# Performance work log

Measured on AMD Instinct MI355X. Metric: run time of the kernel, lower is better.

## Reference

```python
import jax, jax.numpy as jnp
import numpy as np

BETA = 0.5
IGNORE_INDEX = -100
TEMPERATURE = 1.0

N, H, V = 2048, 4096, 32000


def setup_inputs() -> dict:
    key = jax.random.key(0)
    k1, k2, k3, k4, k5 = jax.random.split(key, 5)
    scale_s = 1.0 / np.sqrt(H // 2)
    scale_t = 1.0 / np.sqrt(H)
    return {
        "student": jax.random.normal(k1, (N, H // 2), dtype=jnp.float32),
        "W_s": jax.random.normal(k2, (V, H // 2), dtype=jnp.float32) * scale_s,
        "teacher": jax.random.normal(k3, (N, H), dtype=jnp.float32),
        "W_t": jax.random.normal(k4, (V, H), dtype=jnp.float32) * scale_t,
        "target": jax.random.randint(k5, (N,), 0, V, dtype=jnp.int64),
    }


def reference(student, W_s, teacher, W_t, target):
    # Fused linear + JSD: logits are [N, V] (the huge intermediates Liger avoids
    # materializing by chunking over N).
    s_logits = (student @ W_s.T) / TEMPERATURE          # [N, V]  student -> Q
    t_logits = (teacher @ W_t.T) / TEMPERATURE          # [N, V]  teacher -> P
    log_q = jax.nn.log_softmax(s_logits, axis=-1)
    log_p = jax.nn.log_softmax(t_logits, axis=-1)
    p = jnp.exp(log_p)
    q = jnp.exp(log_q)
    # Generalized JSD(beta): beta*KL(P||M) + (1-beta)*KL(Q||M), M = beta*P + (1-beta)*Q
    m = BETA * p + (1.0 - BETA) * q
    log_m = jnp.log(m)
    per_tok = (BETA * jnp.sum(p * (log_p - log_m), axis=-1)
               + (1.0 - BETA) * jnp.sum(q * (log_q - log_m), axis=-1))  # [N]
    mask = target != IGNORE_INDEX
    n_non_ignore = jnp.maximum(jnp.sum(mask), 1)
    loss = jnp.sum(jnp.where(mask, per_tok, 0.0)) / n_non_ignore.astype(per_tok.dtype)
    return loss
```

## Files before the change

kernel.cpp:

```cpp
#include <hip/hip_runtime.h>
#include <hip/hip_bf16.h>
#include <hip/hip_fp8.h>
#include <stdint.h>

#define BETA 0.5f
#define IGNORE_INDEX (-100)
#define WSCALE 64.0f
#define INV_WSCALE 0.015625f

typedef float f32x4 __attribute__((ext_vector_type(4)));
typedef long longx2 __attribute__((ext_vector_type(2)));

__global__ __launch_bounds__(256) void f32_to_fp8_kernel(
    const float* __restrict__ in, uint8_t* __restrict__ out, int n, float scale) {
  int i = (blockIdx.x * blockDim.x + threadIdx.x) * 8;
  const int stride = gridDim.x * blockDim.x * 8;
  for (; i < n; i += stride) {
    float4 v0 = *reinterpret_cast<const float4*>(in + i);
    float4 v1 = *reinterpret_cast<const float4*>(in + i + 4);
    const float f[8] = {v0.x, v0.y, v0.z, v0.w, v1.x, v1.y, v1.z, v1.w};
    union { uint8_t b[8]; uint2 u; } o;
#pragma unroll
    for (int j = 0; j < 8; ++j) {
      __hip_fp8_e4m3 h(f[j] * scale);
      o.b[j] = h.__x;
    }
    *reinterpret_cast<uint2*>(out + i) = o.u;
  }
}


__global__ __launch_bounds__(512, 2) void gemm_f8q_kernel(
    const uint8_t* __restrict__ At, const uint8_t* __restrict__ Bt,
    uint16_t* __restrict__ Ct, int Kt,
    const uint8_t* __restrict__ As_, const uint8_t* __restrict__ Bs_,
    uint16_t* __restrict__ Cs, int Ks,
    int V, int RT, int CT) {
  __shared__ __align__(16) uint8_t lds[65536];

  const int half = RT * CT;
  const uint8_t *A, *B;
  uint16_t* C;
  int K, bidx = blockIdx.x;
  if (bidx < half) { A = At; B = Bt; C = Ct; K = Kt; }
  else             { A = As_; B = Bs_; C = Cs; K = Ks; bidx -= half; }

  int L = ((half & 7) == 0) ? ((bidx & 7) * (half >> 3) + (bidx >> 3)) : bidx;
  const int rt = L % RT;
  const int ct = L / RT;
  const int row0 = rt * 256;
  const int col0 = ct * 256;

  const int i  = threadIdx.x;
  const int w  = i >> 6;
  const int l  = i & 63;
  const int wl = l & 15;
  const int kg = l >> 4;
  const int wr = w >> 2;
  const int wc = w & 3;

  const int nT = K >> 6;

  const int rg = i >> 2;
  const int pq = i & 3;
  const int qlog = pq ^ ((rg >> 1) & 3);
  const uint8_t* aSrc = A + (size_t)(row0 + rg) * K + qlog * 16;
  const uint8_t* bSrc = B + (size_t)(col0 + rg) * K + qlog * 16;
  uint8_t* ldsu = lds;

#define GL(srcp, dstp)                                                     \
  __builtin_amdgcn_global_load_lds(                                        \
      (const __attribute__((address_space(1))) void*)(srcp),               \
      (__attribute__((address_space(3))) void*)(dstp), 16, 0, 0)

#define STAGE_A(TT)                                                        \
  do {                                                                     \
    const uint8_t* _s = aSrc + (size_t)(TT) * 64;                          \
    uint8_t* _d = ldsu + (((TT) & 1) * 32768) + i * 16;                    \
    GL(_s, _d); GL(_s + (size_t)128 * K, _d + 8192);                       \
  } while (0)

#define STAGE_B(TT)                                                        \
  do {                                                                     \
    const uint8_t* _s = bSrc + (size_t)(TT) * 64;                          \
    uint8_t* _d = ldsu + (((TT) & 1) * 32768) + 16384 + i * 16;            \
    GL(_s, _d); GL(_s + (size_t)128 * K, _d + 8192);                       \
  } while (0)

  int offA[8], offB[4];
  const int qsw = (kg ^ ((wl >> 1) & 3)) * 16;
#pragma unroll
  for (int m = 0; m < 8; ++m) {
    const int r = wr * 128 + m * 16 + wl;
    offA[m] = r * 64 + qsw;
  }
#pragma unroll
  for (int n = 0; n < 4; ++n) {
    const int r = wc * 64 + n * 16 + wl;
    offB[n] = 16384 + r * 64 + qsw;
  }

  f32x4 acc[8][4] = {};
  longx2 af[4], ag[4], bf[4];

  STAGE_A(0); STAGE_B(0);
  if (nT > 1) {
    STAGE_B(1);
    asm volatile("s_waitcnt vmcnt(2)" ::: "memory");
  } else {
    asm volatile("s_waitcnt vmcnt(0)" ::: "memory");
  }
  __builtin_amdgcn_s_barrier();
  __builtin_amdgcn_sched_barrier(0);

  for (int T = 0; T < nT; ++T) {
    const uint8_t* bb = lds + (T & 1) * 32768;
    const bool stg1 = (T + 1) < nT;
    const bool stg2 = (T + 2) < nT;

#pragma unroll
    for (int m = 0; m < 4; ++m)
      af[m] = *reinterpret_cast<const longx2*>(bb + offA[m]);
#pragma unroll
    for (int n = 0; n < 4; ++n)
      bf[n] = *reinterpret_cast<const longx2*>(bb + offB[n]);
    if (stg1) STAGE_A(T + 1);
    __builtin_amdgcn_s_setprio(1);
#pragma unroll
    for (int m = 0; m < 4; ++m)
#pragma unroll
      for (int n = 0; n < 4; ++n)
        acc[m][n] = __builtin_amdgcn_mfma_f32_16x16x32_fp8_fp8(
            af[m][0], bf[n][0], acc[m][n], 0, 0, 0);
    __builtin_amdgcn_s_setprio(0);

#pragma unroll
    for (int m = 0; m < 4; ++m)
      ag[m] = *reinterpret_cast<const longx2*>(bb + offA[4 + m]);
    __builtin_amdgcn_s_setprio(1);
#pragma unroll
    for (int m = 0; m < 4; ++m)
#pragma unroll
      for (int n = 0; n < 4; ++n)
        acc[4 + m][n] = __builtin_amdgcn_mfma_f32_16x16x32_fp8_fp8(
            ag[m][0], bf[n][0], acc[4 + m][n], 0, 0, 0);
    __builtin_amdgcn_s_setprio(0);

    if (stg2) STAGE_B(T + 2);
    __builtin_amdgcn_s_setprio(1);
#pragma unroll
    for (int m = 0; m < 4; ++m)
#pragma unroll
      for (int n = 0; n < 4; ++n)
        acc[m][n] = __builtin_amdgcn_mfma_f32_16x16x32_fp8_fp8(
            af[m][1], bf[n][1], acc[m][n], 0, 0, 0);
    __builtin_amdgcn_s_setprio(0);

    __builtin_amdgcn_s_setprio(1);
#pragma unroll
    for (int m = 0; m < 4; ++m)
#pragma unroll
      for (int n = 0; n < 4; ++n)
        acc[4 + m][n] = __builtin_amdgcn_mfma_f32_16x16x32_fp8_fp8(
            ag[m][1], bf[n][1], acc[4 + m][n], 0, 0, 0);
    __builtin_amdgcn_s_setprio(0);

    if (stg2) {
      asm volatile("s_waitcnt vmcnt(2)" ::: "memory");
    } else {
      asm volatile("s_waitcnt vmcnt(0)" ::: "memory");
    }
    __builtin_amdgcn_s_barrier();
    __builtin_amdgcn_sched_barrier(0);
  }

#pragma unroll
  for (int mg = 0; mg < 8; ++mg)
#pragma unroll
    for (int ng = 0; ng < 4; ++ng)
#pragma unroll
      for (int r = 0; r < 4; ++r) {
        const int row = row0 + wr * 128 + mg * 16 + kg * 4 + r;
        const int col = col0 + wc * 64 + ng * 16 + wl;
        __hip_bfloat16 bv = __float2bfloat16(acc[mg][ng][r] * INV_WSCALE);
        C[(size_t)row * V + col] = *reinterpret_cast<const uint16_t*>(&bv);
      }
#undef STAGE_A
#undef STAGE_B
#undef GL
}

__device__ __forceinline__ void unpack8(uint4 v, float* f) {
  uint32_t w[4] = {v.x, v.y, v.z, v.w};
#pragma unroll
  for (int j = 0; j < 4; ++j) {
    union { uint32_t u; float x; } lo, hi;
    lo.u = (w[j] & 0xffffu) << 16;
    hi.u = w[j] & 0xffff0000u;
    f[2 * j] = lo.x;
    f[2 * j + 1] = hi.x;
  }
}

__device__ __forceinline__ float blockReduce(float v, float* sh) {
#pragma unroll
  for (int o = 32; o >= 1; o >>= 1) v += __shfl_xor(v, o, 64);
  const int w = threadIdx.x >> 6;
  __syncthreads();
  if ((threadIdx.x & 63) == 0) sh[w] = v;
  __syncthreads();
  float r = sh[0];
#pragma unroll
  for (int i = 1; i < 4; ++i) r += sh[i];
  return r;
}

__global__ __launch_bounds__(256) void jsd_rows_kernel(
    const uint16_t* __restrict__ SL, const uint16_t* __restrict__ TL,
    float* __restrict__ per_tok, int V) {
  __shared__ __align__(16) uint16_t rowS[32000];
  __shared__ __align__(16) uint16_t rowT[32000];
  __shared__ float redM[2][4], redS[2][4], red[4];

  const int t = threadIdx.x;
  const int row = blockIdx.x;
  const uint4* gS = reinterpret_cast<const uint4*>(SL + (size_t)row * V);
  const uint4* gT = reinterpret_cast<const uint4*>(TL + (size_t)row * V);
  uint4* lS = reinterpret_cast<uint4*>(rowS);
  uint4* lT = reinterpret_cast<uint4*>(rowT);
  const int nvec = V >> 3;

  float mS = -3.0e38f, sS = 0.f, mT = -3.0e38f, sT = 0.f;
  for (int i = t; i < nvec; i += 256) {
    uint4 vs = gS[i], vt = gT[i];
    lS[i] = vs; lT[i] = vt;
    float fs[8], ft[8];
    unpack8(vs, fs);
    unpack8(vt, ft);
    float vmS = fs[0], vmT = ft[0];
#pragma unroll
    for (int j = 1; j < 8; ++j) { vmS = fmaxf(vmS, fs[j]); vmT = fmaxf(vmT, ft[j]); }
    if (vmS > mS) { sS *= __expf(mS - vmS); mS = vmS; }
    if (vmT > mT) { sT *= __expf(mT - vmT); mT = vmT; }
#pragma unroll
    for (int j = 0; j < 8; ++j) { sS += __expf(fs[j] - mS); sT += __expf(ft[j] - mT); }
  }

#pragma unroll
  for (int o = 32; o >= 1; o >>= 1) {
    float mo = __shfl_xor(mS, o, 64), so = __shfl_xor(sS, o, 64);
    float mn = fmaxf(mS, mo);
    sS = sS * __expf(mS - mn) + so * __expf(mo - mn); mS = mn;
    mo = __shfl_xor(mT, o, 64); so = __shfl_xor(sT, o, 64);
    mn = fmaxf(mT, mo);
    sT = sT * __expf(mT - mn) + so * __expf(mo - mn); mT = mn;
  }
  const int wv = t >> 6;
  if ((t & 63) == 0) {
    redM[0][wv] = mS; redS[0][wv] = sS;
    redM[1][wv] = mT; redS[1][wv] = sT;
  }
  __syncthreads();
  float M0 = redM[0][0], S0 = redS[0][0];
  float M1 = redM[1][0], S1 = redS[1][0];
#pragma unroll
  for (int k = 1; k < 4; ++k) {
    float m2 = redM[0][k], s2 = redS[0][k];
    float mn = fmaxf(M0, m2);
    S0 = S0 * __expf(M0 - mn) + s2 * __expf(m2 - mn); M0 = mn;
    m2 = redM[1][k]; s2 = redS[1][k];
    mn = fmaxf(M1, m2);
    S1 = S1 * __expf(M1 - mn) + s2 * __expf(m2 - mn); M1 = mn;
  }
  const float lseS = M0 + __logf(S0);
  const float lseT = M1 + __logf(S1);

  float acc = 0.f;
  for (int i = t; i < nvec; i += 256) {
    float fs[8], ft[8];
    unpack8(lS[i], fs);
    unpack8(lT[i], ft);
#pragma unroll
    for (int j = 0; j < 8; ++j) {
      const float lq = fs[j] - lseS;
      const float lp = ft[j] - lseT;
      const float q = __expf(lq);
      const float p = __expf(lp);
      const float m = BETA * p + (1.f - BETA) * q;
      const float lm = __logf(m);
      acc += BETA * p * (lp - lm) + (1.f - BETA) * q * (lq - lm);
    }
  }
  acc = blockReduce(acc, red);
  if (t == 0) per_tok[row] = acc;
}

__global__ __launch_bounds__(256) void finalize_kernel(
    const float* __restrict__ per_tok, const int* __restrict__ tgt,
    float* __restrict__ out, int N) {
  __shared__ float redf[4];
  __shared__ int redi[4];
  float s = 0.f;
  int c = 0;
  for (int i = threadIdx.x; i < N; i += 256) {
    if (tgt[i] != IGNORE_INDEX) { s += per_tok[i]; c += 1; }
  }
#pragma unroll
  for (int o = 32; o >= 1; o >>= 1) {
    s += __shfl_xor(s, o, 64);
    c += __shfl_xor(c, o, 64);
  }
  const int w = threadIdx.x >> 6;
  if ((threadIdx.x & 63) == 0) { redf[w] = s; redi[w] = c; }
  __syncthreads();
  if (threadIdx.x == 0) {
    float st = 0.f;
    int ct = 0;
#pragma unroll
    for (int i = 0; i < 4; ++i) { st += redf[i]; ct += redi[i]; }
    out[0] = st / (float)(ct > 0 ? ct : 1);
  }
}

extern "C" void kernel_launch(void* const* d_in, const int* in_sizes, int n_in,
                              void* d_out, int out_size, void* d_ws, size_t ws_size,
                              hipStream_t stream) {
  const float* student = (const float*)d_in[0];
  const float* W_s     = (const float*)d_in[1];
  const float* teacher = (const float*)d_in[2];
  const float* W_t     = (const float*)d_in[3];
  const int*   target  = (const int*)d_in[4];

  const int N  = in_sizes[4];
  const int Hs = in_sizes[0] / N;
  const int Ht = in_sizes[2] / N;
  const int V  = in_sizes[1] / Hs;

  char* ws = (char*)d_ws;
  size_t off = 0;
  auto alloc = [&](size_t bytes) -> void* {
    void* p = ws + off;
    off += (bytes + 255) & ~(size_t)255;
    return p;
  };
  uint8_t* Sf8  = (uint8_t*)alloc((size_t)N * Hs);
  uint8_t* Wsf8 = (uint8_t*)alloc((size_t)V * Hs);
  uint8_t* Tf8  = (uint8_t*)alloc((size_t)N * Ht);
  uint8_t* Wtf8 = (uint8_t*)alloc((size_t)V * Ht);
  uint16_t* slog = (uint16_t*)alloc((size_t)N * V * 2);
  uint16_t* tlog = (uint16_t*)alloc((size_t)N * V * 2);
  float* per_tok = (float*)alloc((size_t)N * sizeof(float));
  (void)ws_size;

  f32_to_fp8_kernel<<<512, 256, 0, stream>>>(student, Sf8, N * Hs, 1.0f);
  f32_to_fp8_kernel<<<2048, 256, 0, stream>>>(W_s, Wsf8, V * Hs, WSCALE);
  f32_to_fp8_kernel<<<512, 256, 0, stream>>>(teacher, Tf8, N * Ht, 1.0f);
  f32_to_fp8_kernel<<<2048, 256, 0, stream>>>(W_t, Wtf8, V * Ht, WSCALE);

  const int RT = N / 256;
  const int CT = V / 256;
  gemm_f8q_kernel<<<2 * RT * CT, 512, 0, stream>>>(
      Tf8, Wtf8, tlog, Ht, Sf8, Wsf8, slog, Hs, V, RT, CT);

  jsd_rows_kernel<<<N, 256, 0, stream>>>(slog, tlog, per_tok, V);
  finalize_kernel<<<1, 256, 0, stream>>>(per_tok, target, (float*)d_out, N);
}
```

Before: 874.1 us.

## Switch FP8 GEMM to scaled MFMA 16x16x128 with K=128 tiles

Replaces the 16x16x32 fp8 MFMA with the MI355 scaled MFMA (16x16x128 f8f6f4), doubling the K tile to 128 and LDS to 128KB double-buffered. The B-operand block scale is folded into the instruction (exponent 2^-6) so the epilogue no longer multiplies by 1/64. This cuts the MFMA instruction count and loop iterations, but the 128KB LDS limits occupancy to one block per CU despite launch_bounds(512,2).

```diff
diff --git a/kernel.cpp b/kernel.cpp
--- a/kernel.cpp
+++ b/kernel.cpp
@@ -6,10 +6,12 @@
 #define BETA 0.5f
 #define IGNORE_INDEX (-100)
 #define WSCALE 64.0f
-#define INV_WSCALE 0.015625f
+#define SCALE_ONE  0x7F7F7F7Fu
+#define SCALE_D64  0x79797979u
 
 typedef float f32x4 __attribute__((ext_vector_type(4)));
-typedef long longx2 __attribute__((ext_vector_type(2)));
+typedef int   i32x4 __attribute__((ext_vector_type(4)));
+typedef int   i32x8 __attribute__((ext_vector_type(8)));
 
 __global__ __launch_bounds__(256) void f32_to_fp8_kernel(
     const float* __restrict__ in, uint8_t* __restrict__ out, int n, float scale) {
@@ -30,13 +32,13 @@
 }
 
 
-__global__ __launch_bounds__(512, 2) void gemm_f8q_kernel(
+__global__ __launch_bounds__(512, 2) void gemm_mx_kernel(
     const uint8_t* __restrict__ At, const uint8_t* __restrict__ Bt,
     uint16_t* __restrict__ Ct, int Kt,
     const uint8_t* __restrict__ As_, const uint8_t* __restrict__ Bs_,
     uint16_t* __restrict__ Cs, int Ks,
     int V, int RT, int CT) {
-  __shared__ __align__(16) uint8_t lds[65536];
+  __shared__ __align__(16) uint8_t lds[131072];
 
   const int half = RT * CT;
   const uint8_t *A, *B;
@@ -59,13 +61,13 @@
   const int wr = w >> 2;
   const int wc = w & 3;
 
-  const int nT = K >> 6;
-
-  const int rg = i >> 2;
-  const int pq = i & 3;
-  const int qlog = pq ^ ((rg >> 1) & 3);
-  const uint8_t* aSrc = A + (size_t)(row0 + rg) * K + qlog * 16;
-  const uint8_t* bSrc = B + (size_t)(col0 + rg) * K + qlog * 16;
+  const int nT = K >> 7;
+
+  const int rg = i >> 3;
+  const int p8 = i & 7;
+  const int qsrc = p8 ^ (rg & 7);
+  const uint8_t* aSrc = A + (size_t)(row0 + rg) * K + qsrc * 16;
+  const uint8_t* bSrc = B + (size_t)(col0 + rg) * K + qsrc * 16;
   uint8_t* ldsu = lds;
 
 #define GL(srcp, dstp)                                                     \
@@ -75,38 +77,55 @@
 
 #define STAGE_A(TT)                                                        \
   do {                                                                     \
-    const uint8_t* _s = aSrc + (size_t)(TT) * 64;                          \
-    uint8_t* _d = ldsu + (((TT) & 1) * 32768) + i * 16;                    \
-    GL(_s, _d); GL(_s + (size_t)128 * K, _d + 8192);                       \
+    const uint8_t* _s = aSrc + (size_t)(TT) * 128;                         \
+    uint8_t* _d = ldsu + (((TT) & 1) * 65536) + i * 16;                    \
+    GL(_s, _d);                                                            \
+    GL(_s + (size_t)64 * K,  _d + 8192);                                   \
+    GL(_s + (size_t)128 * K, _d + 16384);                                  \
+    GL(_s + (size_t)192 * K, _d + 24576);                                  \
   } while (0)
 
 #define STAGE_B(TT)                                                        \
   do {                                                                     \
-    const uint8_t* _s = bSrc + (size_t)(TT) * 64;                          \
-    uint8_t* _d = ldsu + (((TT) & 1) * 32768) + 16384 + i * 16;            \
-    GL(_s, _d); GL(_s + (size_t)128 * K, _d + 8192);                       \
+    const uint8_t* _s = bSrc + (size_t)(TT) * 128;                         \
+    uint8_t* _d = ldsu + (((TT) & 1) * 65536) + 32768 + i * 16;            \
+    GL(_s, _d);                                                            \
+    GL(_s + (size_t)64 * K,  _d + 8192);                                   \
+    GL(_s + (size_t)128 * K, _d + 16384);                                  \
+    GL(_s + (size_t)192 * K, _d + 24576);                                  \
   } while (0)
 
-  int offA[8], offB[4];
-  const int qsw = (kg ^ ((wl >> 1) & 3)) * 16;
+  int offA[8][2], offB[4][2];
 #pragma unroll
   for (int m = 0; m < 8; ++m) {
     const int r = wr * 128 + m * 16 + wl;
-    offA[m] = r * 64 + qsw;
+#pragma unroll
+    for (int s = 0; s < 2; ++s)
+      offA[m][s] = r * 128 + (((2 * kg + s) ^ (wl & 7)) * 16);
   }
 #pragma unroll
   for (int n = 0; n < 4; ++n) {
     const int r = wc * 64 + n * 16 + wl;
-    offB[n] = 16384 + r * 64 + qsw;
+#pragma unroll
+    for (int s = 0; s < 2; ++s)
+      offB[n][s] = 32768 + r * 128 + (((2 * kg + s) ^ (wl & 7)) * 16);
   }
 
   f32x4 acc[8][4] = {};
-  longx2 af[4], ag[4], bf[4];
+  i32x8 aF[4], bF[4];
+
+#define LOADFRAG(dst, base, o0, o1)                                        \
+  do {                                                                     \
+    i32x4 _lo = *reinterpret_cast<const i32x4*>((base) + (o0));            \
+    i32x4 _hi = *reinterpret_cast<const i32x4*>((base) + (o1));            \
+    dst[0] = _lo[0]; dst[1] = _lo[1]; dst[2] = _lo[2]; dst[3] = _lo[3];    \
+    dst[4] = _hi[0]; dst[5] = _hi[1]; dst[6] = _hi[2]; dst[7] = _hi[3];    \
+  } while (0)
 
   STAGE_A(0); STAGE_B(0);
   if (nT > 1) {
     STAGE_B(1);
-    asm volatile("s_waitcnt vmcnt(2)" ::: "memory");
+    asm volatile("s_waitcnt vmcnt(4)" ::: "memory");
   } else {
     asm volatile("s_waitcnt vmcnt(0)" ::: "memory");
   }
@@ -114,59 +133,41 @@
   __builtin_amdgcn_sched_barrier(0);
 
   for (int T = 0; T < nT; ++T) {
-    const uint8_t* bb = lds + (T & 1) * 32768;
+    const uint8_t* bb = lds + (T & 1) * 65536;
     const bool stg1 = (T + 1) < nT;
     const bool stg2 = (T + 2) < nT;
 
 #pragma unroll
     for (int m = 0; m < 4; ++m)
-      af[m] = *reinterpret_cast<const longx2*>(bb + offA[m]);
+      LOADFRAG(aF[m], bb, offA[m][0], offA[m][1]);
 #pragma unroll
     for (int n = 0; n < 4; ++n)
-      bf[n] = *reinterpret_cast<const longx2*>(bb + offB[n]);
+      LOADFRAG(bF[n], bb, offB[n][0], offB[n][1]);
     if (stg1) STAGE_A(T + 1);
     __builtin_amdgcn_s_setprio(1);
 #pragma unroll
     for (int m = 0; m < 4; ++m)
 #pragma unroll
       for (int n = 0; n < 4; ++n)
-        acc[m][n] = __builtin_amdgcn_mfma_f32_16x16x32_fp8_fp8(
-            af[m][0], bf[n][0], acc[m][n], 0, 0, 0);
+        acc[m][n] = __builtin_amdgcn_mfma_scale_f32_16x16x128_f8f6f4(
+            aF[m], bF[n], acc[m][n], 0, 0, 0, SCALE_ONE, 0, SCALE_D64);
     __builtin_amdgcn_s_setprio(0);
 
 #pragma unroll
     for (int m = 0; m < 4; ++m)
-      ag[m] = *reinterpret_cast<const longx2*>(bb + offA[4 + m]);
-    __builtin_amdgcn_s_setprio(1);
-#pragma unroll
-    for (int m = 0; m < 4; ++m)
-#pragma unroll
-      for (int n = 0; n < 4; ++n)
-        acc[4 + m][n] = __builtin_amdgcn_mfma_f32_16x16x32_fp8_fp8(
-            ag[m][0], bf[n][0], acc[4 + m][n], 0, 0, 0);
-    __builtin_amdgcn_s_setprio(0);
-
+      LOADFRAG(aF[m], bb, offA[4 + m][0], offA[4 + m][1]);
     if (stg2) STAGE_B(T + 2);
     __builtin_amdgcn_s_setprio(1);
 #pragma unroll
     for (int m = 0; m < 4; ++m)
 #pragma unroll
       for (int n = 0; n < 4; ++n)
-        acc[m][n] = __builtin_amdgcn_mfma_f32_16x16x32_fp8_fp8(
-            af[m][1], bf[n][1], acc[m][n], 0, 0, 0);
+        acc[4 + m][n] = __builtin_amdgcn_mfma_scale_f32_16x16x128_f8f6f4(
+            aF[m], bF[n], acc[4 + m][n], 0, 0, 0, SCALE_ONE, 0, SCALE_D64);
     __builtin_amdgcn_s_setprio(0);
 
-    __builtin_amdgcn_s_setprio(1);
-#pragma unroll
-    for (int m = 0; m < 4; ++m)
-#pragma unroll
-      for (int n = 0; n < 4; ++n)
-        acc[4 + m][n] = __builtin_amdgcn_mfma_f32_16x16x32_fp8_fp8(
-            ag[m][1], bf[n][1], acc[4 + m][n], 0, 0, 0);
-    __builtin_amdgcn_s_setprio(0);
-
     if (stg2) {
-      asm volatile("s_waitcnt vmcnt(2)" ::: "memory");
+      asm volatile("s_waitcnt vmcnt(4)" ::: "memory");
     } else {
       asm volatile("s_waitcnt vmcnt(0)" ::: "memory");
     }
@@ -182,9 +183,10 @@
       for (int r = 0; r < 4; ++r) {
         const int row = row0 + wr * 128 + mg * 16 + kg * 4 + r;
         const int col = col0 + wc * 64 + ng * 16 + wl;
-        __hip_bfloat16 bv = __float2bfloat16(acc[mg][ng][r] * INV_WSCALE);
+        __hip_bfloat16 bv = __float2bfloat16(acc[mg][ng][r]);
         C[(size_t)row * V + col] = *reinterpret_cast<const uint16_t*>(&bv);
       }
+#undef LOADFRAG
 #undef STAGE_A
 #undef STAGE_B
 #undef GL
@@ -359,7 +361,7 @@
 
   const int RT = N / 256;
   const int CT = V / 256;
-  gemm_f8q_kernel<<<2 * RT * CT, 512, 0, stream>>>(
+  gemm_mx_kernel<<<2 * RT * CT, 512, 0, stream>>>(
       Tf8, Wtf8, tlog, Ht, Sf8, Wsf8, slog, Hs, V, RT, CT);
 
   jsd_rows_kernel<<<N, 256, 0, stream>>>(slog, tlog, per_tok, V);
```

Result: slower. 978.5 us (+11.9%).

## Switch FP8 GEMM to scaled 16x16x128 MFMA with four-stage LDS ring

Applied to the files above, without the earlier changes.

Replaces the 16x16x32 FP8 MFMA inner loop with the MI355X scaled MFMA (16x16x128 f8f6f4). Each instruction covers two 64-wide K tiles, and the weight scale of 1/64 is folded into the hardware scale operand instead of a multiply in the epilogue. LDS grows to 128KB to hold a four-buffer ring, and two tiles are prefetched per iteration. The aim is fewer MFMA issues at higher per-instruction throughput. In exchange, the larger LDS footprint likely limits occupancy to one block per CU despite launch bounds of 2, and the K-fragment packing across buffers has to match the new instruction's operand layout.

```diff
diff --git a/kernel.cpp b/kernel.cpp
--- a/kernel.cpp
+++ b/kernel.cpp
@@ -6,10 +6,12 @@
 #define BETA 0.5f
 #define IGNORE_INDEX (-100)
 #define WSCALE 64.0f
-#define INV_WSCALE 0.015625f
+#define SCALE_ONE  0x7F7F7F7Fu
+#define SCALE_D64  0x79797979u
 
 typedef float f32x4 __attribute__((ext_vector_type(4)));
-typedef long longx2 __attribute__((ext_vector_type(2)));
+typedef int   i32x4 __attribute__((ext_vector_type(4)));
+typedef int   i32x8 __attribute__((ext_vector_type(8)));
 
 __global__ __launch_bounds__(256) void f32_to_fp8_kernel(
     const float* __restrict__ in, uint8_t* __restrict__ out, int n, float scale) {
@@ -30,13 +32,13 @@
 }
 
 
-__global__ __launch_bounds__(512, 2) void gemm_f8q_kernel(
+__global__ __launch_bounds__(512, 2) void gemm_mx2_kernel(
     const uint8_t* __restrict__ At, const uint8_t* __restrict__ Bt,
     uint16_t* __restrict__ Ct, int Kt,
     const uint8_t* __restrict__ As_, const uint8_t* __restrict__ Bs_,
     uint16_t* __restrict__ Cs, int Ks,
     int V, int RT, int CT) {
-  __shared__ __align__(16) uint8_t lds[65536];
+  __shared__ __align__(16) uint8_t lds[131072];
 
   const int half = RT * CT;
   const uint8_t *A, *B;
@@ -59,7 +61,7 @@
   const int wr = w >> 2;
   const int wc = w & 3;
 
-  const int nT = K >> 6;
+  const int nJ = K >> 7;
 
   const int rg = i >> 2;
   const int pq = i & 3;
@@ -76,14 +78,14 @@
 #define STAGE_A(TT)                                                        \
   do {                                                                     \
     const uint8_t* _s = aSrc + (size_t)(TT) * 64;                          \
-    uint8_t* _d = ldsu + (((TT) & 1) * 32768) + i * 16;                    \
+    uint8_t* _d = ldsu + (((TT) & 3) * 32768) + i * 16;                    \
     GL(_s, _d); GL(_s + (size_t)128 * K, _d + 8192);                       \
   } while (0)
 
 #define STAGE_B(TT)                                                        \
   do {                                                                     \
     const uint8_t* _s = bSrc + (size_t)(TT) * 64;                          \
-    uint8_t* _d = ldsu + (((TT) & 1) * 32768) + 16384 + i * 16;            \
+    uint8_t* _d = ldsu + (((TT) & 3) * 32768) + 16384 + i * 16;            \
     GL(_s, _d); GL(_s + (size_t)128 * K, _d + 8192);                       \
   } while (0)
 
@@ -101,72 +103,53 @@
   }
 
   f32x4 acc[8][4] = {};
-  longx2 af[4], ag[4], bf[4];
-
-  STAGE_A(0); STAGE_B(0);
-  if (nT > 1) {
-    STAGE_B(1);
-    asm volatile("s_waitcnt vmcnt(2)" ::: "memory");
+  i32x8 bF[4];
+
+  STAGE_A(0); STAGE_B(0); STAGE_A(1); STAGE_B(1);
+  if (nJ > 1) {
+    STAGE_A(2); STAGE_B(2); STAGE_A(3); STAGE_B(3);
+    asm volatile("s_waitcnt vmcnt(8)" ::: "memory");
   } else {
     asm volatile("s_waitcnt vmcnt(0)" ::: "memory");
   }
   __builtin_amdgcn_s_barrier();
   __builtin_amdgcn_sched_barrier(0);
 
-  for (int T = 0; T < nT; ++T) {
-    const uint8_t* bb = lds + (T & 1) * 32768;
-    const bool stg1 = (T + 1) < nT;
-    const bool stg2 = (T + 2) < nT;
-
-#pragma unroll
-    for (int m = 0; m < 4; ++m)
-      af[m] = *reinterpret_cast<const longx2*>(bb + offA[m]);
-#pragma unroll
-    for (int n = 0; n < 4; ++n)
-      bf[n] = *reinterpret_cast<const longx2*>(bb + offB[n]);
-    if (stg1) STAGE_A(T + 1);
+  for (int j = 0; j < nJ; ++j) {
+    const uint8_t* bufE = lds + ((2 * j) & 3) * 32768;
+    const uint8_t* bufO = lds + ((2 * j + 1) & 3) * 32768;
+    const bool stg2 = (j + 2) < nJ;
+
+#pragma unroll
+    for (int n = 0; n < 4; ++n) {
+      i32x4 be = *reinterpret_cast<const i32x4*>(bufE + offB[n]);
+      i32x4 bo = *reinterpret_cast<const i32x4*>(bufO + offB[n]);
+      bF[n][0] = be[0]; bF[n][1] = be[1]; bF[n][2] = be[2]; bF[n][3] = be[3];
+      bF[n][4] = bo[0]; bF[n][5] = bo[1]; bF[n][6] = bo[2]; bF[n][7] = bo[3];
+    }
+
+    if (stg2) {
+      STAGE_A(2 * j + 4); STAGE_B(2 * j + 4);
+      STAGE_A(2 * j + 5); STAGE_B(2 * j + 5);
+    }
+
     __builtin_amdgcn_s_setprio(1);
 #pragma unroll
-    for (int m = 0; m < 4; ++m)
+    for (int m = 0; m < 8; ++m) {
+      i32x4 ae = *reinterpret_cast<const i32x4*>(bufE + offA[m]);
+      i32x4 ao = *reinterpret_cast<const i32x4*>(bufO + offA[m]);
+      i32x8 aF;
+      aF[0] = ae[0]; aF[1] = ae[1]; aF[2] = ae[2]; aF[3] = ae[3];
+      aF[4] = ao[0]; aF[5] = ao[1]; aF[6] = ao[2]; aF[7] = ao[3];
 #pragma unroll
       for (int n = 0; n < 4; ++n)
-        acc[m][n] = __builtin_amdgcn_mfma_f32_16x16x32_fp8_fp8(
-            af[m][0], bf[n][0], acc[m][n], 0, 0, 0);
+        acc[m][n] = __builtin_amdgcn_mfma_scale_f32_16x16x128_f8f6f4(
+            aF, bF[n], acc[m][n], 0, 0, 0, SCALE_ONE, 0, SCALE_D64);
+    }
     __builtin_amdgcn_s_setprio(0);
 
-#pragma unroll
-    for (int m = 0; m < 4; ++m)
-      ag[m] = *reinterpret_cast<const longx2*>(bb + offA[4 + m]);
-    __builtin_amdgcn_s_setprio(1);
-#pragma unroll
-    for (int m = 0; m < 4; ++m)
-#pragma unroll
-      for (int n = 0; n < 4; ++n)
-        acc[4 + m][n] = __builtin_amdgcn_mfma_f32_16x16x32_fp8_fp8(
-            ag[m][0], bf[n][0], acc[4 + m][n], 0, 0, 0);
-    __builtin_amdgcn_s_setprio(0);
-
-    if (stg2) STAGE_B(T + 2);
-    __builtin_amdgcn_s_setprio(1);
-#pragma unroll
-    for (int m = 0; m < 4; ++m)
-#pragma unroll
-      for (int n = 0; n < 4; ++n)
-        acc[m][n] = __builtin_amdgcn_mfma_f32_16x16x32_fp8_fp8(
-            af[m][1], bf[n][1], acc[m][n], 0, 0, 0);
-    __builtin_amdgcn_s_setprio(0);
-
-    __builtin_amdgcn_s_setprio(1);
-#pragma unroll
-    for (int m = 0; m < 4; ++m)
-#pragma unroll
-      for (int n = 0; n < 4; ++n)
-        acc[4 + m][n] = __builtin_amdgcn_mfma_f32_16x16x32_fp8_fp8(
-            ag[m][1], bf[n][1], acc[4 + m][n], 0, 0, 0);
-    __builtin_amdgcn_s_setprio(0);
-
     if (stg2) {
-      asm volatile("s_waitcnt vmcnt(2)" ::: "memory");
+      asm volatile("s_waitcnt vmcnt(8)" ::: "memory");
     } else {
       asm volatile("s_waitcnt vmcnt(0)" ::: "memory");
     }
@@ -182,7 +165,7 @@
       for (int r = 0; r < 4; ++r) {
         const int row = row0 + wr * 128 + mg * 16 + kg * 4 + r;
         const int col = col0 + wc * 64 + ng * 16 + wl;
-        __hip_bfloat16 bv = __float2bfloat16(acc[mg][ng][r] * INV_WSCALE);
+        __hip_bfloat16 bv = __float2bfloat16(acc[mg][ng][r]);
         C[(size_t)row * V + col] = *reinterpret_cast<const uint16_t*>(&bv);
       }
 #undef STAGE_A
@@ -359,7 +342,7 @@
 
   const int RT = N / 256;
   const int CT = V / 256;
-  gemm_f8q_kernel<<<2 * RT * CT, 512, 0, stream>>>(
+  gemm_mx2_kernel<<<2 * RT * CT, 512, 0, stream>>>(
       Tf8, Wtf8, tlog, Ht, Sf8, Wsf8, slog, Hs, V, RT, CT);
 
   jsd_rows_kernel<<<N, 256, 0, stream>>>(slog, tlog, per_tok, V);
```

After: 753.9 us. -13.8%, faster.
